# Kernel tuning notes

Hardware: AMD Instinct MI355X
Metric: run time of the kernel (lower is better)

Reference implementation:

```python
import jax, jax.numpy as jnp
import numpy as np

EPS = 1e-6
SCAL = 5.0
PARTS = 16
NFEAT = 32
RES = 64


def conv(x, w, b, stride=1):
    y = jax.lax.conv_general_dilated(x, w, (stride, stride), 'SAME',
                                     dimension_numbers=('NCHW', 'OIHW', 'NCHW'))
    return y + b[None, :, None, None]


def spatial_softmax(x):
    b, k, h, w = x.shape
    return jax.nn.softmax(x.reshape(b, k, h * w), axis=-1).reshape(b, k, h, w)


def make_grid(h, w):
    ys = jnp.linspace(-1.0, 1.0, h)
    xs = jnp.linspace(-1.0, 1.0, w)
    gy, gx = jnp.meshgrid(ys, xs, indexing='ij')
    return jnp.stack([gy, gx], axis=-1)  # [h, w, 2]


def e_sigma(x, w1, b1, w2, b2, wp, bp):
    # shared shape/appearance encoder: parts via spatial softmax + residual sum map
    h1 = jax.nn.relu(conv(x, w1, b1, stride=2))   # [B,64,64,64]
    h2 = jax.nn.relu(conv(h1, w2, b2))            # [B,64,64,64]
    parts = spatial_softmax(conv(h2, wp, bp))     # [B,16,64,64]
    return parts, h2


def e_alpha(x, w1, b1, w2, b2):
    h1 = jax.nn.relu(conv(x, w1, b1))
    return conv(h1, w2, b2)                       # [B,32,64,64]


def get_mu_and_prec(parts):
    # soft-argmax mean + 2x2 covariance -> inverse Cholesky factor L_inv
    b, k, h, w = parts.shape
    grid = make_grid(h, w)
    mu = jnp.einsum('bkhw,hwc->bkc', parts, grid)                       # [b,k,2]
    outer = jnp.einsum('hwm,hwn->hwmn', grid, grid)
    cov = jnp.einsum('bkhw,hwmn->bkmn', parts, outer) - jnp.einsum('bkm,bkn->bkmn', mu, mu)
    a = jnp.sqrt(cov[..., 0, 0] + EPS)
    bb = cov[..., 0, 1] / (a + EPS)
    c = jnp.sqrt(jnp.maximum(cov[..., 1, 1] - bb * bb, 0.0) + EPS)
    det = a * c
    z = jnp.zeros_like(a)
    L_inv = SCAL / (det[..., None, None] + EPS) * jnp.stack(
        [jnp.stack([c, z], axis=-1), jnp.stack([-bb, a], axis=-1)], axis=-2)  # [b,k,2,2]
    return mu, L_inv


def feat_mu_to_enc(alpha, mu, L_inv, h, w):
    # render Cauchy-shaped part heatmaps from (mu, L_inv) and paint part features
    grid = make_grid(h, w)
    dist = grid[None, None] - mu[:, :, None, None, :]        # [b,k,h,w,2]
    proj = jnp.einsum('bkhwi,bkij->bkhwj', dist, L_inv)
    heat = 1.0 / (1.0 + jnp.sum(proj * proj, axis=-1))       # [b,k,h,w]
    norm = heat / (jnp.sum(heat, axis=(2, 3), keepdims=True) + EPS)
    fmap = jnp.einsum('bkf,bkhw->bfhw', alpha, norm)         # [b,nf,h,w]
    return jnp.concatenate([heat, fmap], axis=1)             # [b,nk+nf,h,w]


def decoder(enc, w1, b1, w2, b2, w3, b3):
    h1 = jax.nn.relu(conv(enc, w1, b1))                      # [B,64,64,64]
    up = jnp.repeat(jnp.repeat(h1, 2, axis=2), 2, axis=3)    # nearest upsample -> 128
    h2 = jax.nn.relu(conv(up, w2, b2))
    return jax.nn.sigmoid(conv(h2, w3, b3))                  # [B,3,128,128]


def setup_inputs():
    key = jax.random.key(0)
    ks = jax.random.split(key, 16)
    def w(k, shape):
        fan_in = shape[1] * shape[2] * shape[3]
        return (jax.random.normal(k, shape, jnp.float32) / np.sqrt(fan_in)).astype(jnp.float32)
    B = 32
    return {
        'x': jax.random.uniform(ks[0], (B, 3, 128, 128), jnp.float32),
        'x_spatial_transform': jax.random.uniform(ks[1], (B, 3, 128, 128), jnp.float32),
        'x_appearance_transform': jax.random.uniform(ks[2], (B, 3, 128, 128), jnp.float32),
        'coord': jax.random.normal(ks[3], (B, PARTS, 2), jnp.float32) * 0.5,
        'vector': jax.random.normal(ks[4], (B, PARTS, 2), jnp.float32) * 0.1,
        'es_w1': w(ks[5], (RES, 3, 3, 3)), 'es_b1': jnp.zeros((RES,), jnp.float32),
        'es_w2': w(ks[6], (RES, RES, 3, 3)), 'es_b2': jnp.zeros((RES,), jnp.float32),
        'es_wp': w(ks[7], (PARTS, RES, 3, 3)), 'es_bp': jnp.zeros((PARTS,), jnp.float32),
        'ea_w1': w(ks[8], (RES, RES, 3, 3)), 'ea_b1': jnp.zeros((RES,), jnp.float32),
        'ea_w2': w(ks[9], (NFEAT, RES, 3, 3)), 'ea_b2': jnp.zeros((NFEAT,), jnp.float32),
        'd_w1': w(ks[10], (RES, PARTS + NFEAT, 3, 3)), 'd_b1': jnp.zeros((RES,), jnp.float32),
        'd_w2': w(ks[11], (32, RES, 3, 3)), 'd_b2': jnp.zeros((32,), jnp.float32),
        'd_w3': w(ks[12], (3, 32, 3, 3)), 'd_b3': jnp.zeros((3,), jnp.float32),
    }


def reference(x, x_spatial_transform, x_appearance_transform, coord, vector,
              es_w1, es_b1, es_w2, es_b2, es_wp, es_bp,
              ea_w1, ea_b1, ea_w2, ea_b2,
              d_w1, d_b1, d_w2, d_b2, d_w3, d_b3):
    # shape stream (appearance-transformed image -> geometry)
    shape_parts, _ = e_sigma(x_appearance_transform, es_w1, es_b1, es_w2, es_b2, es_wp, es_bp)
    mu, L_inv = get_mu_and_prec(shape_parts)
    # appearance stream (spatially-transformed image -> appearance)
    app_parts, app_sum = e_sigma(x_spatial_transform, es_w1, es_b1, es_w2, es_b2, es_wp, es_bp)
    f_xs = e_alpha(app_sum, ea_w1, ea_b1, ea_w2, ea_b2)
    # local part appearances: gather features under each part map
    alpha = jnp.einsum('bfhw,bkhw->bkf', f_xs, app_parts)
    encoding = feat_mu_to_enc(alpha, mu, L_inv, 64, 64)
    reconstruction = decoder(encoding, d_w1, d_b1, d_w2, d_b2, d_w3, d_b3)
    # composite loss
    mu_a, L_inv_a = get_mu_and_prec(app_parts)
    rec_loss = jnp.mean((x - reconstruction) ** 2)
    equiv_loss = jnp.mean((mu - mu_a) ** 2) + 0.01 * jnp.mean((L_inv - L_inv_a) ** 2)
    transport_loss = jnp.mean((mu_a - (coord + vector)) ** 2)
    loss = rec_loss + equiv_loss + transport_loss
    return reconstruction, loss
```

## Files before the change

### kernel.cpp

```cpp
#include <hip/hip_runtime.h>
#include <hip/hip_bf16.h>

#define EPS 1e-6f
#define SCAL 5.0f

typedef __attribute__((ext_vector_type(8))) short bf8v;
typedef __attribute__((ext_vector_type(4))) float f32x4;

#define OFF_MU     0
#define OFF_LINV   1024
#define OFF_MUA    3072
#define OFF_LINVA  4096
#define OFF_HSUM   6144
#define OFF_ALPHA  6656
#define OFF_REC    23040
#define OFF_R1     32768
#define OFF_R2     (OFF_R1 + 8388608)
#define OFF_R3     (OFF_R2 + 8388608)
#define WS_TOTAL   (OFF_R3 + 16777216)

#define BA_XA   ((size_t)2 * OFF_R3)
#define BA_X2   ((size_t)2 * OFF_R1)
#define OFF_PARTSF OFF_R2
#define OFF_PROBS  (OFF_R2 + 4194304)
#define BA_EA1  ((size_t)2 * OFF_R3)
#define OFF_FXS (OFF_R3 + 4194304)
#define BA_E    ((size_t)2 * OFF_R2)
#define BA_D1   ((size_t)2 * OFF_R1)
#define BA_D2   ((size_t)2 * OFF_R3)

#define WT_ESW1 0
#define WT_ESB1 1728
#define WT_ESB2 1792
#define WT_ESBP 1856
#define WT_EAB1 1872
#define WT_EAB2 1936
#define WT_DB1  1968
#define WT_DB2  2032
#define WT_W3P  2064
#define WT_DB3  2928
#define P_WP2  0
#define P_WPP  36864
#define P_WPA1 46080
#define P_WPA2 82944
#define P_WPD1 101376
#define P_WPD2 138240

__device__ __attribute__((aligned(16))) float g_ws[WS_TOTAL];
__device__ __attribute__((aligned(16))) float g_wt[3072];
__device__ __attribute__((aligned(16))) __hip_bfloat16 g_wp[156672];
__device__ int g_isbf16;

__device__ __forceinline__ float selz(bool c, float v) { return c ? v : 0.f; }
__device__ __forceinline__ float cvtbf(short s) {
    return __uint_as_float(((unsigned int)(unsigned short)s) << 16);
}
__device__ __forceinline__ short f2bf(float f) {
    unsigned u = __float_as_uint(f);
    u += 0x7fff + ((u >> 16) & 1);
    return (short)(u >> 16);
}
__device__ __forceinline__ float ldin(const void* p, size_t i, int bf) {
    return bf ? __bfloat162float(((const __hip_bfloat16*)p)[i])
              : ((const float*)p)[i];
}

__device__ __forceinline__ float block_sum(float v) {
    __shared__ float sb[8];
    for (int off = 32; off; off >>= 1) v += __shfl_down(v, off, 64);
    int lane = threadIdx.x & 63, wid = threadIdx.x >> 6;
    __syncthreads();
    if (lane == 0) sb[wid] = v;
    __syncthreads();
    float r = 0.f;
    for (int i = 0; i < 4; ++i) r += sb[i];
    return r;
}
__device__ __forceinline__ float block_max(float v) {
    __shared__ float sb[8];
    for (int off = 32; off; off >>= 1) v = fmaxf(v, __shfl_down(v, off, 64));
    int lane = threadIdx.x & 63, wid = threadIdx.x >> 6;
    __syncthreads();
    if (lane == 0) sb[wid] = v;
    __syncthreads();
    float r = -1e30f;
    for (int i = 0; i < 4; ++i) r = fmaxf(r, sb[i]);
    return r;
}

__global__ void detect_k(const void* x) {
    const __hip_bfloat16* p = (const __hip_bfloat16*)x;
    int lane = threadIdx.x & 63;
    float v = 0.f;
    for (int i = lane; i < 256; i += 64) {
        float a = fabsf(__bfloat162float(p[i]));
        if (!(a <= 2.0f)) v = 1.f;
    }
    for (int off = 32; off; off >>= 1) v += __shfl_down(v, off, 64);
    if (lane == 0) {
        g_isbf16 = (v == 0.f) ? 1 : 0;
        g_ws[OFF_REC] = 0.f;
    }
}

__global__ void wpack_k(const void* esw1, const void* esb1, const void* esw2, const void* esb2,
                        const void* eswp, const void* esbp, const void* eaw1, const void* eab1,
                        const void* eaw2, const void* eab2, const void* dw1, const void* db1,
                        const void* dw2, const void* db2, const void* dw3, const void* db3) {
    int bf = g_isbf16;
    int gid0 = blockIdx.x * 256 + threadIdx.x, stride = gridDim.x * 256;
    for (int g = gid0; g < 512; g += stride) g_ws[OFF_HSUM + g] = 0.f;
    for (int g = gid0; g < 1728; g += stride) g_wt[WT_ESW1 + g] = ldin(esw1, g, bf);
    for (int g = gid0; g < 64; g += stride) g_wt[WT_ESB1 + g] = ldin(esb1, g, bf);
    for (int g = gid0; g < 64; g += stride) g_wt[WT_ESB2 + g] = ldin(esb2, g, bf);
    for (int g = gid0; g < 16; g += stride) g_wt[WT_ESBP + g] = ldin(esbp, g, bf);
    for (int g = gid0; g < 64; g += stride) g_wt[WT_EAB1 + g] = ldin(eab1, g, bf);
    for (int g = gid0; g < 32; g += stride) g_wt[WT_EAB2 + g] = ldin(eab2, g, bf);
    for (int g = gid0; g < 64; g += stride) g_wt[WT_DB1 + g] = ldin(db1, g, bf);
    for (int g = gid0; g < 32; g += stride) g_wt[WT_DB2 + g] = ldin(db2, g, bf);
    for (int g = gid0; g < 3; g += stride) g_wt[WT_DB3 + g] = ldin(db3, g, bf);
    for (int g = gid0; g < 864; g += stride) {
        int t = g / 96, o = (g / 32) % 3, k = g & 31;
        g_wt[WT_W3P + g] = ldin(dw3, (size_t)(o * 32 + k) * 9 + t, bf);
    }
    for (int g = gid0; g < 36864; g += stride) {
        int t = g >> 12, n = (g >> 6) & 63, k = g & 63;
        g_wp[P_WP2 + g] = __float2bfloat16(ldin(esw2, (size_t)(n * 64 + k) * 9 + t, bf));
    }
    for (int g = gid0; g < 9216; g += stride) {
        int t = g >> 10, n = (g >> 6) & 15, k = g & 63;
        g_wp[P_WPP + g] = __float2bfloat16(ldin(eswp, (size_t)(n * 64 + k) * 9 + t, bf));
    }
    for (int g = gid0; g < 36864; g += stride) {
        int t = g >> 12, n = (g >> 6) & 63, k = g & 63;
        g_wp[P_WPA1 + g] = __float2bfloat16(ldin(eaw1, (size_t)(n * 64 + k) * 9 + t, bf));
    }
    for (int g = gid0; g < 18432; g += stride) {
        int t = g >> 11, n = (g >> 6) & 31, k = g & 63;
        g_wp[P_WPA2 + g] = __float2bfloat16(ldin(eaw2, (size_t)(n * 64 + k) * 9 + t, bf));
    }
    for (int g = gid0; g < 36864; g += stride) {
        int t = g >> 12, n = (g >> 6) & 63, k = g & 63;
        float v = (k < 48) ? ldin(dw1, (size_t)(n * 48 + k) * 9 + t, bf) : 0.f;
        g_wp[P_WPD1 + g] = __float2bfloat16(v);
    }
    for (int g = gid0; g < 18432; g += stride) {
        int t = g >> 11, n = (g >> 6) & 31, k = g & 63;
        g_wp[P_WPD2 + g] = __float2bfloat16(ldin(dw2, (size_t)(n * 64 + k) * 9 + t, bf));
    }
}

__global__ void __launch_bounds__(256)
conv_s2n_k(const void* __restrict__ inA, const void* __restrict__ inB) {
    int bf = g_isbf16;
    int tile = blockIdx.x & 15;
    int gb = blockIdx.x >> 4;
    int g = gb & 3, b = gb >> 2;
    const void* in = (b < 32) ? inA : inB;
    int bb = b & 31;
    int pix = tile * 256 + threadIdx.x;
    int y = pix >> 6, x = pix & 63;
    size_t inb = (size_t)bb * 3 * 16384;
    const float* W = g_wt + WT_ESW1 + (size_t)(g * 16) * 27;
    float acc[16];
    #pragma unroll
    for (int o = 0; o < 16; ++o) acc[o] = g_wt[WT_ESB1 + g * 16 + o];
    int iy0 = 2 * y, ix0 = 2 * x;
    bool my2 = (iy0 + 2 < 128), mx2 = (ix0 + 2 < 128);
    int iy2 = my2 ? iy0 + 2 : 127, ix2 = mx2 ? ix0 + 2 : 127;
    for (int ic = 0; ic < 3; ++ic) {
        size_t pb = inb + ic * 16384;
        float t[9];
        t[0] = ldin(in, pb + iy0 * 128 + ix0, bf);
        t[1] = ldin(in, pb + iy0 * 128 + ix0 + 1, bf);
        t[2] = selz(mx2, ldin(in, pb + iy0 * 128 + ix2, bf));
        t[3] = ldin(in, pb + (iy0 + 1) * 128 + ix0, bf);
        t[4] = ldin(in, pb + (iy0 + 1) * 128 + ix0 + 1, bf);
        t[5] = selz(mx2, ldin(in, pb + (iy0 + 1) * 128 + ix2, bf));
        t[6] = selz(my2, ldin(in, pb + iy2 * 128 + ix0, bf));
        t[7] = selz(my2, ldin(in, pb + iy2 * 128 + ix0 + 1, bf));
        t[8] = selz(my2 && mx2, ldin(in, pb + iy2 * 128 + ix2, bf));
        #pragma unroll
        for (int o = 0; o < 16; ++o) {
            const float* wr = W + (o * 3 + ic) * 9;
            float a = acc[o];
            #pragma unroll
            for (int j = 0; j < 9; ++j) a = fmaf(t[j], wr[j], a);
            acc[o] = a;
        }
    }
    __hip_bfloat16* out = (__hip_bfloat16*)g_ws + BA_XA + ((size_t)b * 4096 + pix) * 64 + g * 16;
    #pragma unroll
    for (int o = 0; o < 16; ++o) out[o] = __float2bfloat16(fmaxf(acc[o], 0.f));
}

template<int TR>
__device__ __forceinline__ void stage_tile(__hip_bfloat16* sA,
                                           const __hip_bfloat16* __restrict__ inb, int y0) {
    for (int g = threadIdx.x; g < TR * 512; g += 256) {
        int r = g >> 9;
        int rem = g & 511;
        int px = rem >> 3, j = rem & 7;
        int yy = y0 - 1 + r;
        int P = px + 1;
        bf8v v = (bf8v){0, 0, 0, 0, 0, 0, 0, 0};
        if (yy >= 0 && yy <= 63)
            v = *(const bf8v*)(inb + ((size_t)(yy * 64 + px) * 64 + j * 8));
        *(bf8v*)(sA + ((r * 66 + P) * 64 + ((j ^ (P & 7)) * 8))) = v;
    }
    if (threadIdx.x < TR * 16) {
        int g = threadIdx.x;
        int r = g >> 4, rem = g & 15, side = rem >> 3, j = rem & 7;
        int P = side ? 65 : 0;
        *(bf8v*)(sA + ((r * 66 + P) * 64 + ((j ^ (P & 7)) * 8))) = (bf8v){0, 0, 0, 0, 0, 0, 0, 0};
    }
}

template<int MS>
__device__ __forceinline__ void ld_a(const __hip_bfloat16* sA, int it, int rowIn,
                                     int l15, int quad, bf8v (&a)[MS]) {
    const int t = it >> 1, c = it & 1;
    const int dy = t / 3 - 1, dx = t % 3 - 1;
    const int r = rowIn + 1 + dy;
    const int j = c * 4 + quad;
    #pragma unroll
    for (int ms = 0; ms < MS; ++ms) {
        int P = ms * 16 + l15 + dx + 1;
        a[ms] = *(const bf8v*)(sA + ((r * 66 + P) * 64 + ((j ^ (P & 7)) * 8)));
    }
}
template<int MS>
__device__ __forceinline__ void ld_a2(const __hip_bfloat16* sA, int it, int rowbase,
                                      int l15, int quad, bf8v (&a)[2][MS]) {
    const int t = it >> 1, c = it & 1;
    const int dy = t / 3 - 1, dx = t % 3 - 1;
    const int j = c * 4 + quad;
    #pragma unroll
    for (int rp = 0; rp < 2; ++rp) {
        const int r = rowbase + rp + 1 + dy;
        #pragma unroll
        for (int ms = 0; ms < MS; ++ms) {
            int P = ms * 16 + l15 + dx + 1;
            a[rp][ms] = *(const bf8v*)(sA + ((r * 66 + P) * 64 + ((j ^ (P & 7)) * 8)));
        }
    }
}
template<int TOTN, int NS>
__device__ __forceinline__ void ld_b(int it, int ocoff, int l15, int quad, int wp_off,
                                     bf8v (&bv)[NS]) {
    const int t = it >> 1, c = it & 1;
    #pragma unroll
    for (int ns = 0; ns < NS; ++ns)
        bv[ns] = *(const bf8v*)(g_wp + wp_off +
                 ((size_t)(t * TOTN + ocoff + ns * 16 + l15) * 64 + c * 32 + quad * 8));
}

template<int TOTN, int NS, int MS>
__device__ __forceinline__ void conv_body(const __hip_bfloat16* sA, int rowIn,
                                          int l15, int quad, int wp_off,
                                          f32x4 (&acc)[MS][NS]) {
    bf8v bq[3][NS];
    bf8v a[2][MS];
    ld_b<TOTN, NS>(0, 0, l15, quad, wp_off, bq[0]);
    ld_b<TOTN, NS>(1, 0, l15, quad, wp_off, bq[1]);
    ld_a<MS>(sA, 0, rowIn, l15, quad, a[0]);
    #pragma unroll
    for (int it = 0; it < 18; ++it) {
        if (it + 2 < 18) ld_b<TOTN, NS>(it + 2, 0, l15, quad, wp_off, bq[(it + 2) % 3]);
        if (it + 1 < 18) ld_a<MS>(sA, it + 1, rowIn, l15, quad, a[(it + 1) & 1]);
        #pragma unroll
        for (int ns = 0; ns < NS; ++ns)
            #pragma unroll
            for (int ms = 0; ms < MS; ++ms)
                acc[ms][ns] = __builtin_amdgcn_mfma_f32_16x16x32_bf16(
                    a[it & 1][ms], bq[it % 3][ns], acc[ms][ns], 0, 0, 0);
    }
}

template<int TOTN, int NSW, int MS>
__device__ __forceinline__ void conv_body2(const __hip_bfloat16* sA, int rowbase, int ocoff,
                                           int l15, int quad, int wp_off,
                                           f32x4 (&acc)[2][MS][NSW]) {
    bf8v bq[3][NSW];
    bf8v a[2][2][MS];
    ld_b<TOTN, NSW>(0, ocoff, l15, quad, wp_off, bq[0]);
    ld_b<TOTN, NSW>(1, ocoff, l15, quad, wp_off, bq[1]);
    ld_a2<MS>(sA, 0, rowbase, l15, quad, a[0]);
    #pragma unroll
    for (int it = 0; it < 18; ++it) {
        if (it + 2 < 18) ld_b<TOTN, NSW>(it + 2, ocoff, l15, quad, wp_off, bq[(it + 2) % 3]);
        if (it + 1 < 18) ld_a2<MS>(sA, it + 1, rowbase, l15, quad, a[(it + 1) & 1]);
        #pragma unroll
        for (int rp = 0; rp < 2; ++rp)
            #pragma unroll
            for (int ns = 0; ns < NSW; ++ns)
                #pragma unroll
                for (int ms = 0; ms < MS; ++ms)
                    acc[rp][ms][ns] = __builtin_amdgcn_mfma_f32_16x16x32_bf16(
                        a[it & 1][rp][ms], bq[it % 3][ns], acc[rp][ms][ns], 0, 0, 0);
    }
}

template<int TOTN, int NS, int OUTF32, int RELU>
__device__ __forceinline__ void epi_std(f32x4 (&acc)[4][NS], int bO, int y,
                                        int l15, int quad, int bias_off, size_t out_off) {
    #pragma unroll
    for (int ns = 0; ns < NS; ++ns) {
        float bias = g_wt[bias_off + ns * 16 + l15];
        #pragma unroll
        for (int ms = 0; ms < 4; ++ms) {
            #pragma unroll
            for (int r = 0; r < 4; ++r) {
                int pix = ms * 16 + quad * 4 + r;
                float v = acc[ms][ns][r] + bias;
                if (RELU) v = fmaxf(v, 0.f);
                size_t o = out_off + ((size_t)(bO * 4096 + y * 64 + pix)) * TOTN + ns * 16 + l15;
                if (OUTF32) g_ws[o] = v;
                else ((__hip_bfloat16*)g_ws)[o] = __float2bfloat16(v);
            }
        }
    }
}
template<int TOTN, int NSW, int OUTF32, int RELU>
__device__ __forceinline__ void epi_2r(f32x4 (&acc)[2][4][NSW], int bO, int y0, int rowbase,
                                       int ocoff, int l15, int quad, int bias_off,
                                       size_t out_off) {
    #pragma unroll
    for (int rp = 0; rp < 2; ++rp) {
        int y = y0 + rowbase + rp;
        #pragma unroll
        for (int ns = 0; ns < NSW; ++ns) {
            float bias = g_wt[bias_off + ocoff + ns * 16 + l15];
            #pragma unroll
            for (int ms = 0; ms < 4; ++ms) {
                #pragma unroll
                for (int r = 0; r < 4; ++r) {
                    int pix = ms * 16 + quad * 4 + r;
                    float v = acc[rp][ms][ns][r] + bias;
                    if (RELU) v = fmaxf(v, 0.f);
                    size_t o = out_off + ((size_t)(bO * 4096 + y * 64 + pix)) * TOTN +
                               ocoff + ns * 16 + l15;
                    if (OUTF32) g_ws[o] = v;
                    else ((__hip_bfloat16*)g_ws)[o] = __float2bfloat16(v);
                }
            }
        }
    }
}

template<int TOTN, int NSW, int OUTF32, int RELU>
__global__ void __launch_bounds__(256) __attribute__((amdgpu_waves_per_eu(2, 3)))
conv_mfl_k(size_t in_off, int wp_off, int bias_off, size_t out_off) {
    __shared__ __hip_bfloat16 sA[6 * 66 * 64];
    int wid = threadIdx.x >> 6, lane = threadIdx.x & 63;
    int l15 = lane & 15, quad = lane >> 4;
    int b = blockIdx.x >> 4, y0 = (blockIdx.x & 15) * 4;
    int og = wid & 1, rowbase = (wid >> 1) * 2;
    int ocoff = og * NSW * 16;
    const __hip_bfloat16* inb = (const __hip_bfloat16*)g_ws + in_off + (size_t)b * 4096 * 64;
    stage_tile<6>(sA, inb, y0);
    __syncthreads();
    f32x4 acc[2][4][NSW];
    #pragma unroll
    for (int rp = 0; rp < 2; ++rp)
        #pragma unroll
        for (int ms = 0; ms < 4; ++ms)
            #pragma unroll
            for (int ns = 0; ns < NSW; ++ns) acc[rp][ms][ns] = (f32x4){0.f, 0.f, 0.f, 0.f};
    conv_body2<TOTN, NSW, 4>(sA, rowbase, ocoff, l15, quad, wp_off, acc);
    epi_2r<TOTN, NSW, OUTF32, RELU>(acc, b, y0, rowbase, ocoff, l15, quad, bias_off, out_off);
}

__global__ void __launch_bounds__(256) __attribute__((amdgpu_waves_per_eu(2, 3)))
conv_pea_k() {
    __shared__ __hip_bfloat16 sA[6 * 66 * 64];
    int wid = threadIdx.x >> 6, lane = threadIdx.x & 63;
    int l15 = lane & 15, quad = lane >> 4;
    int b = blockIdx.x >> 4, y0 = (blockIdx.x & 15) * 4;
    int y = y0 + wid;
    const __hip_bfloat16* inb = (const __hip_bfloat16*)g_ws + BA_X2 + (size_t)b * 4096 * 64;
    stage_tile<6>(sA, inb, y0);
    __syncthreads();
    f32x4 accP[4][1];
    #pragma unroll
    for (int ms = 0; ms < 4; ++ms) accP[ms][0] = (f32x4){0.f, 0.f, 0.f, 0.f};
    conv_body<16, 1, 4>(sA, wid, l15, quad, P_WPP, accP);
    epi_std<16, 1, 1, 0>(accP, b, y, l15, quad, WT_ESBP, (size_t)OFF_PARTSF);
    if (b >= 32) {
        int og = wid & 1, rowbase = (wid >> 1) * 2;
        int ocoff = og * 32;
        f32x4 accE[2][4][2];
        #pragma unroll
        for (int rp = 0; rp < 2; ++rp)
            #pragma unroll
            for (int ms = 0; ms < 4; ++ms)
                #pragma unroll
                for (int ns = 0; ns < 2; ++ns) accE[rp][ms][ns] = (f32x4){0.f, 0.f, 0.f, 0.f};
        conv_body2<64, 2, 4>(sA, rowbase, ocoff, l15, quad, P_WPA1, accE);
        epi_2r<64, 2, 0, 1>(accE, b - 32, y0, rowbase, ocoff, l15, quad, WT_EAB1, BA_EA1);
    }
}

__global__ void __launch_bounds__(256) __attribute__((amdgpu_waves_per_eu(2, 3)))
conv_upmf2_k(size_t in_off, int wp_off, int bias_off, size_t out_off) {
    __shared__ __hip_bfloat16 sA[4 * 66 * 64];
    int wid = threadIdx.x >> 6, lane = threadIdx.x & 63;
    int l15 = lane & 15, quad = lane >> 4;
    int b = blockIdx.x >> 5, y0 = (blockIdx.x & 31) * 4;
    int ri0 = (y0 >> 1) - 1;
    const __hip_bfloat16* inb = (const __hip_bfloat16*)g_ws + in_off + (size_t)b * 4096 * 64;
    for (int g = threadIdx.x; g < 2048; g += 256) {
        int r = g >> 9;
        int rem = g & 511;
        int px = rem >> 3, j = rem & 7;
        int yi = ri0 + r;
        int P = px + 1;
        bf8v v = (bf8v){0, 0, 0, 0, 0, 0, 0, 0};
        if (yi >= 0 && yi <= 63)
            v = *(const bf8v*)(inb + ((size_t)(yi * 64 + px) * 64 + j * 8));
        *(bf8v*)(sA + ((r * 66 + P) * 64 + ((j ^ (P & 7)) * 8))) = v;
    }
    if (threadIdx.x < 64) {
        int g = threadIdx.x;
        int r = g >> 4, rem = g & 15, side = rem >> 3, j = rem & 7;
        int P = side ? 65 : 0;
        *(bf8v*)(sA + ((r * 66 + P) * 64 + ((j ^ (P & 7)) * 8))) = (bf8v){0, 0, 0, 0, 0, 0, 0, 0};
    }
    __syncthreads();
    int og = wid & 1, rowbase = (wid >> 1) * 2;
    f32x4 acc[2][8];
    #pragma unroll
    for (int rp = 0; rp < 2; ++rp)
        #pragma unroll
        for (int ms = 0; ms < 8; ++ms) acc[rp][ms] = (f32x4){0.f, 0.f, 0.f, 0.f};
    bf8v bq[3][1];
    ld_b<32, 1>(0, og * 16, l15, quad, wp_off, bq[0]);
    ld_b<32, 1>(1, og * 16, l15, quad, wp_off, bq[1]);
    #pragma unroll
    for (int it = 0; it < 18; ++it) {
        if (it + 2 < 18) ld_b<32, 1>(it + 2, og * 16, l15, quad, wp_off, bq[(it + 2) % 3]);
        const int t = it >> 1, c = it & 1;
        const int dy = t / 3 - 1, dx = t % 3 - 1;
        #pragma unroll
        for (int rp = 0; rp < 2; ++rp) {
            int yy = y0 + rowbase + rp + dy;
            if (yy >= 0 && yy <= 127) {
                int r = (yy >> 1) - ri0;
                int j = c * 4 + quad;
                bf8v a[8];
                #pragma unroll
                for (int ms = 0; ms < 8; ++ms) {
                    int xx = ms * 16 + l15 + dx;
                    int P = (xx < 0) ? 0 : ((xx > 127) ? 65 : ((xx >> 1) + 1));
                    a[ms] = *(const bf8v*)(sA + ((r * 66 + P) * 64 + ((j ^ (P & 7)) * 8)));
                }
                #pragma unroll
                for (int ms = 0; ms < 8; ++ms)
                    acc[rp][ms] = __builtin_amdgcn_mfma_f32_16x16x32_bf16(a[ms], bq[it % 3][0], acc[rp][ms], 0, 0, 0);
            }
        }
    }
    float bias = g_wt[bias_off + og * 16 + l15];
    #pragma unroll
    for (int rp = 0; rp < 2; ++rp) {
        int y = y0 + rowbase + rp;
        #pragma unroll
        for (int ms = 0; ms < 8; ++ms) {
            #pragma unroll
            for (int r = 0; r < 4; ++r) {
                int pix = ms * 16 + quad * 4 + r;
                float v = fmaxf(acc[rp][ms][r] + bias, 0.f);
                size_t o = out_off + ((size_t)(b * 16384 + y * 128 + pix)) * 32 + og * 16 + l15;
                ((__hip_bfloat16*)g_ws)[o] = __float2bfloat16(v);
            }
        }
    }
}

__global__ void sm_mom3_k() {
    int bk = blockIdx.x;
    int b = bk >> 4, k = bk & 15;
    int app = (b >= 32);
    const float* P = g_ws + OFF_PARTSF + (size_t)b * 4096 * 16 + k;
    float r[16];
    #pragma unroll
    for (int j = 0; j < 16; ++j) r[j] = P[(size_t)(threadIdx.x + j * 256) * 16];
    float m = r[0];
    #pragma unroll
    for (int j = 1; j < 16; ++j) m = fmaxf(m, r[j]);
    m = block_max(m);
    float s = 0.f;
    #pragma unroll
    for (int j = 0; j < 16; ++j) { r[j] = __expf(r[j] - m); s += r[j]; }
    s = block_sum(s);
    float inv = 1.0f / s;
    float sy = 0, sx = 0, syy = 0, sxy = 0, sxx = 0;
    #pragma unroll
    for (int j = 0; j < 16; ++j) {
        float pv = r[j] * inv;
        int i = threadIdx.x + j * 256;
        if (app) g_ws[OFF_PROBS + ((size_t)(b - 32) * 16 + k) * 4096 + i] = pv;
        float gy = -1.0f + (i >> 6) * (2.0f / 63.0f);
        float gx = -1.0f + (i & 63) * (2.0f / 63.0f);
        sy += pv * gy; sx += pv * gx;
        syy += pv * gy * gy; sxy += pv * gy * gx; sxx += pv * gx * gx;
    }
    sy = block_sum(sy); sx = block_sum(sx);
    syy = block_sum(syy); sxy = block_sum(sxy); sxx = block_sum(sxx);
    if (threadIdx.x == 0) {
        float c00 = syy - sy * sy, c01 = sxy - sy * sx, c11 = sxx - sx * sx;
        float a = sqrtf(fmaxf(c00 + EPS, 1e-12f));
        float bb = c01 / (a + EPS);
        float cc = sqrtf(fmaxf(c11 - bb * bb, 0.f) + EPS);
        float det = a * cc;
        float sc = SCAL / (det + EPS);
        int idx = app ? ((b - 32) * 16 + k) : (b * 16 + k);
        int mu_off = app ? OFF_MUA : OFF_MU;
        int linv_off = app ? OFF_LINVA : OFF_LINV;
        g_ws[mu_off + idx * 2 + 0] = sy;
        g_ws[mu_off + idx * 2 + 1] = sx;
        g_ws[linv_off + idx * 4 + 0] = cc * sc;
        g_ws[linv_off + idx * 4 + 1] = 0.f;
        g_ws[linv_off + idx * 4 + 2] = -bb * sc;
        g_ws[linv_off + idx * 4 + 3] = a * sc;
    }
}

__global__ void alpha2_k() {
    int b = blockIdx.x & 31, k = blockIdx.x >> 5;
    int bk = b * 16 + k;
    __shared__ float pl[4096];
    const float* pr = g_ws + OFF_PROBS + (size_t)bk * 4096;
    for (int i = threadIdx.x; i < 4096; i += 256) pl[i] = pr[i];
    __syncthreads();
    float acc[32];
    #pragma unroll
    for (int f = 0; f < 32; ++f) acc[f] = 0.f;
    for (int i = threadIdx.x; i < 4096; i += 256) {
        float pv = pl[i];
        const float* fp = g_ws + OFF_FXS + (size_t)(b * 4096 + i) * 32;
        #pragma unroll
        for (int f = 0; f < 32; ++f) acc[f] = fmaf(pv, fp[f], acc[f]);
    }
    __shared__ float sw[4][32];
    int lane = threadIdx.x & 63, wid = threadIdx.x >> 6;
    #pragma unroll
    for (int f = 0; f < 32; ++f)
        for (int off = 32; off; off >>= 1) acc[f] += __shfl_down(acc[f], off, 64);
    if (lane == 0) {
        #pragma unroll
        for (int f = 0; f < 32; ++f) sw[wid][f] = acc[f];
    }
    __syncthreads();
    if (threadIdx.x < 32)
        g_ws[OFF_ALPHA + bk * 32 + threadIdx.x] =
            sw[0][threadIdx.x] + sw[1][threadIdx.x] + sw[2][threadIdx.x] + sw[3][threadIdx.x];
}

__global__ void heat2_k() {
    int tile = blockIdx.x & 15, b = blockIdx.x >> 4;
    __shared__ float hs[16];
    if (threadIdx.x < 16) hs[threadIdx.x] = 0.f;
    __syncthreads();
    int pix = tile * 256 + threadIdx.x;
    float gy = -1.0f + (pix >> 6) * (2.0f / 63.0f);
    float gx = -1.0f + (pix & 63) * (2.0f / 63.0f);
    bf8v e0, e1;
    float hv[16];
    #pragma unroll
    for (int k = 0; k < 16; ++k) {
        int bk = b * 16 + k;
        float m0 = g_ws[OFF_MU + bk * 2], m1 = g_ws[OFF_MU + bk * 2 + 1];
        float L00 = g_ws[OFF_LINV + bk * 4 + 0], L10 = g_ws[OFF_LINV + bk * 4 + 2],
              L11 = g_ws[OFF_LINV + bk * 4 + 3];
        float d0 = gy - m0, d1 = gx - m1;
        float p0 = d0 * L00 + d1 * L10;
        float p1 = d1 * L11;
        float h = 1.0f / (1.0f + p0 * p0 + p1 * p1);
        hv[k] = h;
        short sbits = f2bf(h);
        if (k < 8) e0[k] = sbits; else e1[k - 8] = sbits;
    }
    __hip_bfloat16* E = (__hip_bfloat16*)g_ws + BA_E + (size_t)(b * 4096 + pix) * 64;
    *(bf8v*)E = e0;
    *(bf8v*)(E + 8) = e1;
    #pragma unroll
    for (int k = 0; k < 16; ++k) {
        float v = hv[k];
        for (int off = 32; off; off >>= 1) v += __shfl_down(v, off, 64);
        if ((threadIdx.x & 63) == 0) atomicAdd(&hs[k], v);
    }
    __syncthreads();
    if (threadIdx.x < 16)
        atomicAdd(&g_ws[OFF_HSUM + b * 16 + threadIdx.x], hs[threadIdx.x]);
}

__global__ void fmap2_k() {
    int tile = blockIdx.x & 15, b = blockIdx.x >> 4;
    __shared__ float coef[16][32];
    for (int i = threadIdx.x; i < 512; i += 256) {
        int k = i >> 5, f = i & 31;
        coef[k][f] = g_ws[OFF_ALPHA + (b * 16 + k) * 32 + f] /
                     (g_ws[OFF_HSUM + b * 16 + k] + EPS);
    }
    __syncthreads();
    int pix = tile * 256 + threadIdx.x;
    __hip_bfloat16* E = (__hip_bfloat16*)g_ws + BA_E + (size_t)(b * 4096 + pix) * 64;
    float h[16];
    #pragma unroll
    for (int k = 0; k < 16; ++k) h[k] = __bfloat162float(E[k]);
    #pragma unroll
    for (int f = 0; f < 32; ++f) {
        float a = 0.f;
        #pragma unroll
        for (int k = 0; k < 16; ++k) a = fmaf(h[k], coef[k][f], a);
        E[16 + f] = __float2bfloat16(a);
    }
    #pragma unroll
    for (int z = 48; z < 64; ++z) E[z] = __float2bfloat16(0.f);
}

__global__ void __launch_bounds__(256)
conv_sign_k(const void* __restrict__ ximg, void* __restrict__ outp) {
    int bf = g_isbf16;
    int tile = blockIdx.x & 63, b = blockIdx.x >> 6;
    int pix = tile * 256 + threadIdx.x;
    int y = pix >> 7, x = pix & 127;
    const short* D2 = (const short*)((const __hip_bfloat16*)g_ws + BA_D2 + (size_t)b * 16384 * 32);
    float acc[3];
    #pragma unroll
    for (int o = 0; o < 3; ++o) acc[o] = g_wt[WT_DB3 + o];
    #pragma unroll
    for (int t = 0; t < 9; ++t) {
        int dy = t / 3 - 1, dx = t % 3 - 1;
        int yy = y + dy, xx = x + dx;
        if (yy < 0 || yy > 127 || xx < 0 || xx > 127) continue;
        const short* sp = D2 + (size_t)(yy * 128 + xx) * 32;
        #pragma unroll
        for (int c = 0; c < 4; ++c) {
            bf8v v = *(const bf8v*)(sp + c * 8);
            #pragma unroll
            for (int j = 0; j < 8; ++j) {
                float av = cvtbf(v[j]);
                int k = c * 8 + j;
                acc[0] = fmaf(av, g_wt[WT_W3P + (t * 3 + 0) * 32 + k], acc[0]);
                acc[1] = fmaf(av, g_wt[WT_W3P + (t * 3 + 1) * 32 + k], acc[1]);
                acc[2] = fmaf(av, g_wt[WT_W3P + (t * 3 + 2) * 32 + k], acc[2]);
            }
        }
    }
    float es = 0.f;
    #pragma unroll
    for (int o = 0; o < 3; ++o) {
        float v = 1.0f / (1.0f + __expf(-acc[o]));
        size_t oidx = ((size_t)b * 3 + o) * 16384 + pix;
        if (bf) ((__hip_bfloat16*)outp)[oidx] = __float2bfloat16(v);
        else    ((float*)outp)[oidx] = v;
        float e = ldin(ximg, oidx, bf) - v;
        es += e * e;
    }
    float s = block_sum(es);
    if (threadIdx.x == 0) atomicAdd(&g_ws[OFF_REC], s);
}

__global__ void loss_k(const void* __restrict__ coord,
                       const void* __restrict__ vec,
                       void* __restrict__ outp) {
    int bf = g_isbf16;
    const float* mu = g_ws + OFF_MU;
    const float* linv = g_ws + OFF_LINV;
    const float* mu_a = g_ws + OFF_MUA;
    const float* linv_a = g_ws + OFF_LINVA;
    float s1 = 0, s2 = 0, s3 = 0;
    for (int i = threadIdx.x; i < 1024; i += 256) {
        float d = mu[i] - mu_a[i];
        s1 += d * d;
        float t = ldin(coord, i, bf) + ldin(vec, i, bf);
        float d3 = mu_a[i] - t;
        s3 += d3 * d3;
    }
    for (int i = threadIdx.x; i < 2048; i += 256) {
        float d = linv[i] - linv_a[i];
        s2 += d * d;
    }
    s1 = block_sum(s1);
    s2 = block_sum(s2);
    s3 = block_sum(s3);
    if (threadIdx.x == 0) {
        float loss = g_ws[OFF_REC] / 1572864.0f + s1 / 1024.0f + 0.01f * (s2 / 2048.0f)
                   + s3 / 1024.0f;
        if (bf) ((__hip_bfloat16*)outp)[1572864] = __float2bfloat16(loss);
        else    ((float*)outp)[1572864] = loss;
    }
}

extern "C" void kernel_launch(void* const* d_in, const int* in_sizes, int n_in,
                              void* d_out, int out_size, void* d_ws, size_t ws_size,
                              hipStream_t stream) {
    const void* x     = d_in[0];
    const void* x_st  = d_in[1];
    const void* x_at  = d_in[2];
    const void* coord = d_in[3];
    const void* vec   = d_in[4];

    dim3 blk(256);

    detect_k<<<1, 64, 0, stream>>>(x);
    wpack_k<<<64, blk, 0, stream>>>(
        d_in[5],  d_in[6],  d_in[7],  d_in[8],
        d_in[9],  d_in[10], d_in[11], d_in[12],
        d_in[13], d_in[14], d_in[15], d_in[16],
        d_in[17], d_in[18], d_in[19], d_in[20]);

    conv_s2n_k<<<64 * 4 * 16, blk, 0, stream>>>(x_at, x_st);
    conv_mfl_k<64, 2, 0, 1><<<1024, blk, 0, stream>>>(BA_XA, P_WP2, WT_ESB2, BA_X2);

    conv_pea_k<<<1024, blk, 0, stream>>>();
    sm_mom3_k<<<1024, blk, 0, stream>>>();

    conv_mfl_k<32, 1, 1, 0><<<512, blk, 0, stream>>>(BA_EA1, P_WPA2, WT_EAB2, (size_t)OFF_FXS);
    alpha2_k<<<512, blk, 0, stream>>>();

    heat2_k<<<512, blk, 0, stream>>>();
    fmap2_k<<<512, blk, 0, stream>>>();

    conv_mfl_k<64, 2, 0, 1><<<512, blk, 0, stream>>>(BA_E, P_WPD1, WT_DB1, BA_D1);
    conv_upmf2_k<<<1024, blk, 0, stream>>>(BA_D1, P_WPD2, WT_DB2, BA_D2);
    conv_sign_k<<<32 * 64, blk, 0, stream>>>(x, d_out);

    loss_k<<<1, blk, 0, stream>>>(coord, vec, d_out);
}
```

Measured before the change: 403.9 us.

## Store part logits planar via LDS transpose; batch-major block order; prefetch decoder taps

The part-logit conv epilogue now stages its accumulators in shared memory and writes the logits in a planar [b,k,h*w] layout with vectorized float4 stores, instead of scattered per-element stores with a 16-float stride. The softmax/moment kernel then reads each part map contiguously rather than at stride 16. The conv block index is remapped so consecutive blocks cover different batch items at the same row band. The final decoder conv issues all nine tap loads per channel chunk before the FMAs, using clamped addresses and zero select, to raise memory-level parallelism. This costs extra syncthreads and LDS traffic in the conv kernel.

```diff
diff --git a/kernel.cpp b/kernel.cpp
--- a/kernel.cpp
+++ b/kernel.cpp
@@ -301,26 +301,6 @@
     }
 }
 
-template<int TOTN, int NS, int OUTF32, int RELU>
-__device__ __forceinline__ void epi_std(f32x4 (&acc)[4][NS], int bO, int y,
-                                        int l15, int quad, int bias_off, size_t out_off) {
-    #pragma unroll
-    for (int ns = 0; ns < NS; ++ns) {
-        float bias = g_wt[bias_off + ns * 16 + l15];
-        #pragma unroll
-        for (int ms = 0; ms < 4; ++ms) {
-            #pragma unroll
-            for (int r = 0; r < 4; ++r) {
-                int pix = ms * 16 + quad * 4 + r;
-                float v = acc[ms][ns][r] + bias;
-                if (RELU) v = fmaxf(v, 0.f);
-                size_t o = out_off + ((size_t)(bO * 4096 + y * 64 + pix)) * TOTN + ns * 16 + l15;
-                if (OUTF32) g_ws[o] = v;
-                else ((__hip_bfloat16*)g_ws)[o] = __float2bfloat16(v);
-            }
-        }
-    }
-}
 template<int TOTN, int NSW, int OUTF32, int RELU>
 __device__ __forceinline__ void epi_2r(f32x4 (&acc)[2][4][NSW], int bO, int y0, int rowbase,
                                        int ocoff, int l15, int quad, int bias_off,
@@ -376,8 +356,8 @@
     __shared__ __hip_bfloat16 sA[6 * 66 * 64];
     int wid = threadIdx.x >> 6, lane = threadIdx.x & 63;
     int l15 = lane & 15, quad = lane >> 4;
-    int b = blockIdx.x >> 4, y0 = (blockIdx.x & 15) * 4;
-    int y = y0 + wid;
+    int b = blockIdx.x & 63;
+    int y0 = (int)(blockIdx.x >> 6) * 4;
     const __hip_bfloat16* inb = (const __hip_bfloat16*)g_ws + BA_X2 + (size_t)b * 4096 * 64;
     stage_tile<6>(sA, inb, y0);
     __syncthreads();
@@ -385,7 +365,6 @@
     #pragma unroll
     for (int ms = 0; ms < 4; ++ms) accP[ms][0] = (f32x4){0.f, 0.f, 0.f, 0.f};
     conv_body<16, 1, 4>(sA, wid, l15, quad, P_WPP, accP);
-    epi_std<16, 1, 1, 0>(accP, b, y, l15, quad, WT_ESBP, (size_t)OFF_PARTSF);
     if (b >= 32) {
         int og = wid & 1, rowbase = (wid >> 1) * 2;
         int ocoff = og * 32;
@@ -399,6 +378,21 @@
         conv_body2<64, 2, 4>(sA, rowbase, ocoff, l15, quad, P_WPA1, accE);
         epi_2r<64, 2, 0, 1>(accE, b - 32, y0, rowbase, ocoff, l15, quad, WT_EAB1, BA_EA1);
     }
+    __syncthreads();
+    float* tb = (float*)sA;
+    float biasP = g_wt[WT_ESBP + l15];
+    #pragma unroll
+    for (int ms = 0; ms < 4; ++ms)
+        #pragma unroll
+        for (int r = 0; r < 4; ++r)
+            tb[l15 * 260 + wid * 64 + ms * 16 + quad * 4 + r] = accP[ms][0][r] + biasP;
+    __syncthreads();
+    int k = threadIdx.x >> 4, xo = (threadIdx.x & 15) * 16;
+    float* dst = g_ws + OFF_PARTSF + ((size_t)(b * 16 + k)) * 4096 + y0 * 64 + xo;
+    const float* src = tb + k * 260 + xo;
+    #pragma unroll
+    for (int i = 0; i < 16; i += 4)
+        *(f32x4*)(dst + i) = *(const f32x4*)(src + i);
 }
 
 __global__ void __launch_bounds__(256) __attribute__((amdgpu_waves_per_eu(2, 3)))
@@ -479,12 +473,12 @@
 
 __global__ void sm_mom3_k() {
     int bk = blockIdx.x;
-    int b = bk >> 4, k = bk & 15;
+    int b = bk >> 4;
     int app = (b >= 32);
-    const float* P = g_ws + OFF_PARTSF + (size_t)b * 4096 * 16 + k;
+    const float* P = g_ws + OFF_PARTSF + (size_t)bk * 4096;
     float r[16];
     #pragma unroll
-    for (int j = 0; j < 16; ++j) r[j] = P[(size_t)(threadIdx.x + j * 256) * 16];
+    for (int j = 0; j < 16; ++j) r[j] = P[threadIdx.x + j * 256];
     float m = r[0];
     #pragma unroll
     for (int j = 1; j < 16; ++j) m = fmaxf(m, r[j]);
@@ -499,7 +493,7 @@
     for (int j = 0; j < 16; ++j) {
         float pv = r[j] * inv;
         int i = threadIdx.x + j * 256;
-        if (app) g_ws[OFF_PROBS + ((size_t)(b - 32) * 16 + k) * 4096 + i] = pv;
+        if (app) g_ws[OFF_PROBS + (size_t)(bk - 512) * 4096 + i] = pv;
         float gy = -1.0f + (i >> 6) * (2.0f / 63.0f);
         float gx = -1.0f + (i & 63) * (2.0f / 63.0f);
         sy += pv * gy; sx += pv * gx;
@@ -514,7 +508,7 @@
         float cc = sqrtf(fmaxf(c11 - bb * bb, 0.f) + EPS);
         float det = a * cc;
         float sc = SCAL / (det + EPS);
-        int idx = app ? ((b - 32) * 16 + k) : (b * 16 + k);
+        int idx = app ? (bk - 512) : bk;
         int mu_off = app ? OFF_MUA : OFF_MU;
         int linv_off = app ? OFF_LINVA : OFF_LINV;
         g_ws[mu_off + idx * 2 + 0] = sy;
@@ -630,22 +624,28 @@
     float acc[3];
     #pragma unroll
     for (int o = 0; o < 3; ++o) acc[o] = g_wt[WT_DB3 + o];
-    #pragma unroll
-    for (int t = 0; t < 9; ++t) {
-        int dy = t / 3 - 1, dx = t % 3 - 1;
-        int yy = y + dy, xx = x + dx;
-        if (yy < 0 || yy > 127 || xx < 0 || xx > 127) continue;
-        const short* sp = D2 + (size_t)(yy * 128 + xx) * 32;
-        #pragma unroll
-        for (int c = 0; c < 4; ++c) {
-            bf8v v = *(const bf8v*)(sp + c * 8);
+    const bf8v zv = (bf8v){0, 0, 0, 0, 0, 0, 0, 0};
+    #pragma unroll
+    for (int c = 0; c < 4; ++c) {
+        bf8v v[9];
+        #pragma unroll
+        for (int t = 0; t < 9; ++t) {
+            int dy = t / 3 - 1, dx = t % 3 - 1;
+            int yy = y + dy, xx = x + dx;
+            bool ok = ((unsigned)yy < 128u) && ((unsigned)xx < 128u);
+            int ys = ok ? yy : y, xs = ok ? xx : x;
+            bf8v tmp = *(const bf8v*)(D2 + (size_t)(ys * 128 + xs) * 32 + c * 8);
+            v[t] = ok ? tmp : zv;
+        }
+        #pragma unroll
+        for (int t = 0; t < 9; ++t) {
             #pragma unroll
             for (int j = 0; j < 8; ++j) {
-                float av = cvtbf(v[j]);
-                int k = c * 8 + j;
-                acc[0] = fmaf(av, g_wt[WT_W3P + (t * 3 + 0) * 32 + k], acc[0]);
-                acc[1] = fmaf(av, g_wt[WT_W3P + (t * 3 + 1) * 32 + k], acc[1]);
-                acc[2] = fmaf(av, g_wt[WT_W3P + (t * 3 + 2) * 32 + k], acc[2]);
+                float av = cvtbf(v[t][j]);
+                int kk = c * 8 + j;
+                acc[0] = fmaf(av, g_wt[WT_W3P + (t * 3 + 0) * 32 + kk], acc[0]);
+                acc[1] = fmaf(av, g_wt[WT_W3P + (t * 3 + 1) * 32 + kk], acc[1]);
+                acc[2] = fmaf(av, g_wt[WT_W3P + (t * 3 + 2) * 32 + kk], acc[2]);
             }
         }
     }
```

New measurement: 437.2 us. 8.3% more time.
